# Kernel optimization log

Measured on AMD Instinct MI355X. Metric: run time of the kernel, lower is better.

Reference implementation:

```python
import jax, jax.numpy as jnp
import numpy as np
from jax import lax

B_J0 = 0.01   # config.b_j0
R_M = 1.0     # config.R_m
BETA = 1.8    # isAdapt=1 branch
GAMMA = 0.5   # config.gamma
LENS = 0.5    # config.lens
SCALE = 6.0   # config.scale
HIGHT = 0.15  # config.hight


def _gauss(x, mu, sigma):
    return jnp.exp(-(x - mu) ** 2 / (2.0 * sigma ** 2)) / jnp.sqrt(2.0 * jnp.pi) / sigma


@jax.custom_vjp
def spike_fn(x):
    return (x > 0).astype(x.dtype)

def _spike_fwd(x):
    return spike_fn(x), x

def _spike_bwd(x, g):
    # 'MG' multi-gaussian surrogate gradient from ActFun_adp.backward
    temp = (_gauss(x, 0.0, LENS) * (1.0 + HIGHT)
            - _gauss(x, LENS, SCALE * LENS) * HIGHT
            - _gauss(x, -LENS, SCALE * LENS) * HIGHT)
    return (g * temp * GAMMA,)

spike_fn.defvjp(_spike_fwd, _spike_bwd)


def setup_inputs() -> dict:
    key = jax.random.key(0)
    ks = jax.random.split(key, 20)
    B, T, I, H, O = 256, 250, 700, 128, 20
    def xav(k, shape):
        lim = jnp.sqrt(6.0 / (shape[0] + shape[1]))
        return jax.random.uniform(k, shape, jnp.float32, -lim, lim)
    def orth(k, n):
        a = jax.random.normal(k, (n, n), jnp.float32)
        q, r = jnp.linalg.qr(a)
        return q * jnp.sign(jnp.diag(r))[None, :]
    return {
        'input': jax.random.normal(ks[0], (B, T, I), jnp.float32),
        'A1_mask': jnp.ones((H, H), jnp.float32),
        'A2_mask': jnp.ones((H, H), jnp.float32),
        'W_ih1': xav(ks[1], (H, I)), 'b_ih1': jnp.zeros((H,), jnp.float32),
        'W_h1h1': orth(ks[2], H), 'b_h1h1': jnp.zeros((H,), jnp.float32),
        'W_h1h2': xav(ks[3], (H, H)), 'b_h1h2': jnp.zeros((H,), jnp.float32),
        'W_h2h2': orth(ks[4], H), 'b_h2h2': jnp.zeros((H,), jnp.float32),
        'W_h2o': xav(ks[5], (O, H)), 'b_h2o': jnp.zeros((O,), jnp.float32),
        'tau_adp_h1': 150.0 + 10.0 * jax.random.normal(ks[6], (H,), jnp.float32),
        'tau_adp_h2': 150.0 + 10.0 * jax.random.normal(ks[7], (H,), jnp.float32),
        'tau_m_h1': 20.0 + 5.0 * jax.random.normal(ks[8], (H,), jnp.float32),
        'tau_m_h2': 20.0 + 5.0 * jax.random.normal(ks[9], (H,), jnp.float32),
        'tau_m_o': 20.0 + 5.0 * jax.random.normal(ks[10], (O,), jnp.float32),
        'hid1_mem0': jax.random.uniform(ks[11], (B, H), jnp.float32),
        'hid2_mem0': jax.random.uniform(ks[12], (B, H), jnp.float32),
        'out_mem0': jax.random.uniform(ks[13], (B, O), jnp.float32),
    }


def reference(input, A1_mask, A2_mask,
              W_ih1, b_ih1, W_h1h1, b_h1h1, W_h1h2, b_h1h2,
              W_h2h2, b_h2h2, W_h2o, b_h2o,
              tau_adp_h1, tau_adp_h2, tau_m_h1, tau_m_h2, tau_m_o,
              hid1_mem0, hid2_mem0, out_mem0):
    B, T, _ = input.shape
    H = W_ih1.shape[0]
    O = W_h2o.shape[0]
    # time-constant decays (dt = 1), computed once
    a1 = jnp.exp(-1.0 / tau_m_h1)
    r1 = jnp.exp(-1.0 / tau_adp_h1)
    a2 = jnp.exp(-1.0 / tau_m_h2)
    r2 = jnp.exp(-1.0 / tau_adp_h2)
    ao = jnp.exp(-1.0 / tau_m_o)

    xT = jnp.swapaxes(input, 0, 1)  # [T, B, I]
    carry0 = (hid1_mem0, jnp.zeros((B, H), input.dtype), jnp.full((B, H), B_J0, input.dtype),
              hid2_mem0, jnp.zeros((B, H), input.dtype), jnp.full((B, H), B_J0, input.dtype),
              out_mem0, jnp.zeros((B, O), input.dtype))

    def step(carry, xs):
        x_t, t = xs
        h1m, h1s, b1, h2m, h2s, b2, om, acc = carry
        # layer 1: input + recurrent drive, adaptive threshold LIF update
        in1 = x_t @ W_ih1.T + b_ih1 + h1s @ W_h1h1.T + b_h1h1
        b1 = r1 * b1 + (1.0 - r1) * h1s
        Bth1 = B_J0 + BETA * b1
        h1m = h1m * a1 + (1.0 - a1) * R_M * in1 - Bth1 * h1s
        h1s = spike_fn(h1m - Bth1)
        # layer 2
        in2 = h1s @ W_h1h2.T + b_h1h2 + h2s @ W_h2h2.T + b_h2h2
        b2 = r2 * b2 + (1.0 - r2) * h2s
        Bth2 = B_J0 + BETA * b2
        h2m = h2m * a2 + (1.0 - a2) * R_M * in2 - Bth2 * h2s
        h2s = spike_fn(h2m - Bth2)
        # leaky-integrator readout (no spike)
        om = om * ao + (1.0 - ao) * R_M * (h2s @ W_h2o.T + b_h2o)
        # accumulate softmax only for t > 10
        acc = acc + jnp.where(t > 10, 1.0, 0.0) * jax.nn.softmax(om, axis=1)
        return (h1m, h1s, b1, h2m, h2s, b2, om, acc), None

    final, _ = lax.scan(step, carry0, (xT, jnp.arange(T)))
    output = final[-1]
    A_norm = jnp.sum(jnp.abs(W_h1h1)) + jnp.sum(jnp.abs(W_h2h2))
    return output, A_norm


if __name__ == '__main__':
    out = reference(**setup_inputs())
    print(out[0].shape, out[1])
```

## Files before the change

kernel.cpp:

```cpp
#include <hip/hip_runtime.h>
#include <hip/hip_bf16.h>
#include <stdint.h>

#define HN 128
#define TSTEPS 250
#define ON 20
#define GK 700
#define NKT 22

typedef _Float16 h2 __attribute__((ext_vector_type(2)));
typedef _Float16 h8 __attribute__((ext_vector_type(8)));
typedef float f4 __attribute__((ext_vector_type(4)));

__device__ __forceinline__ h2 bch_u(uint32_t u) { return __builtin_bit_cast(h2, u); }
__device__ __forceinline__ h2 bch_f(float f)    { return __builtin_bit_cast(h2, f); }
__device__ __forceinline__ float fdot2(h2 a, h2 b, float c) {
    return __builtin_amdgcn_fdot2(a, b, c, false);
}
__device__ __forceinline__ float pack2(float x, float y) {
    h2 p; p.x = (_Float16)x; p.y = (_Float16)y;
    return __builtin_bit_cast(float, p);
}
__device__ __forceinline__ uint32_t pack2u(float x, float y) {
    h2 p; p.x = (_Float16)x; p.y = (_Float16)y;
    return __builtin_bit_cast(uint32_t, p);
}

__global__ __launch_bounds__(256) void ff_gemm(const float* __restrict__ X,
                                               const float* __restrict__ W,
                                               const float* __restrict__ bias,
                                               float* __restrict__ out) {
    __shared__ __align__(16) uint32_t Xs[2][128][16];
    __shared__ __align__(16) uint32_t Ws[2][128][16];
    const int tid   = threadIdx.x;
    const int w     = tid >> 6;
    const int lane  = tid & 63;
    const int m0    = blockIdx.x * 128;
    const int srow  = tid & 127;
    const int shalf = tid >> 7;
    const int lr    = lane & 15;
    const int lg    = lane >> 4;

    f4 acc[2][8];
#pragma unroll
    for (int m = 0; m < 2; ++m)
#pragma unroll
        for (int n = 0; n < 8; ++n) acc[m][n] = (f4){0.f, 0.f, 0.f, 0.f};

    float4 x4[4], w4[4];

#define LOADT(t)                                                               \
    {                                                                          \
        const int k0 = (t) * 32 + shalf * 16;                                  \
        if ((t) < 21 || shalf == 0) {                                          \
            _Pragma("unroll")                                                  \
            for (int q = 0; q < 4; ++q) {                                      \
                x4[q] = *(const float4*)&X[(size_t)(m0 + srow) * GK + k0 + q * 4]; \
                w4[q] = *(const float4*)&W[(size_t)srow * GK + k0 + q * 4];    \
            }                                                                  \
        } else {       \
            _Pragma("unroll")                                                  \
            for (int q = 0; q < 3; ++q) {                                      \
                x4[q] = *(const float4*)&X[(size_t)(m0 + srow) * GK + k0 + q * 4]; \
                w4[q] = *(const float4*)&W[(size_t)srow * GK + k0 + q * 4];    \
            }                                                                  \
            x4[3] = (float4){0.f, 0.f, 0.f, 0.f};                              \
            w4[3] = (float4){0.f, 0.f, 0.f, 0.f};                              \
        }                                                                      \
    }
#define STORET(buf)                                                            \
    {                                                                          \
        _Pragma("unroll")                                                      \
        for (int q = 0; q < 4; ++q) {                                          \
            Xs[buf][srow][shalf * 8 + 2 * q]     = pack2u(x4[q].x, x4[q].y);   \
            Xs[buf][srow][shalf * 8 + 2 * q + 1] = pack2u(x4[q].z, x4[q].w);   \
            Ws[buf][srow][shalf * 8 + 2 * q]     = pack2u(w4[q].x, w4[q].y);   \
            Ws[buf][srow][shalf * 8 + 2 * q + 1] = pack2u(w4[q].z, w4[q].w);   \
        }                                                                      \
    }

    LOADT(0);
    STORET(0);
    __syncthreads();
    int cur = 0;
    for (int t = 0; t < NKT; ++t) {
        if (t + 1 < NKT) LOADT(t + 1);
        h8 a[2];
#pragma unroll
        for (int m = 0; m < 2; ++m) {
            const uint4 au = *(const uint4*)&Xs[cur][w * 32 + m * 16 + lr][lg * 4];
            a[m] = __builtin_bit_cast(h8, au);
        }
#pragma unroll
        for (int n = 0; n < 8; ++n) {
            const uint4 bu = *(const uint4*)&Ws[cur][n * 16 + lr][lg * 4];
            const h8 bf = __builtin_bit_cast(h8, bu);
            acc[0][n] = __builtin_amdgcn_mfma_f32_16x16x32_f16(a[0], bf, acc[0][n], 0, 0, 0);
            acc[1][n] = __builtin_amdgcn_mfma_f32_16x16x32_f16(a[1], bf, acc[1][n], 0, 0, 0);
        }
        if (t + 1 < NKT) STORET(cur ^ 1);
        __syncthreads();
        cur ^= 1;
    }

    float bv[8];
#pragma unroll
    for (int n = 0; n < 8; ++n) bv[n] = bias[n * 16 + lr];
#pragma unroll
    for (int m = 0; m < 2; ++m)
#pragma unroll
        for (int q = 0; q < 4; ++q) {
            const size_t row = (size_t)(m0 + w * 32 + m * 16 + lg * 4 + q);
#pragma unroll
            for (int n = 0; n < 8; ++n)
                out[row * HN + n * 16 + lr] = acc[m][n][q] + bv[n];
        }
#undef LOADT
#undef STORET
}

__device__ __forceinline__ float mv1h(const float4 (&WP)[16][HN],
                                      const uint4 (&sv)[16], int j) {
    float a0 = 0.f, a1 = 0.f, a2 = 0.f, a3 = 0.f;
#pragma unroll
    for (int t = 0; t < 16; ++t) {
        const float4 wl = WP[t][j];
        const uint4  s  = sv[t];
        a0 = fdot2(bch_f(wl.x), bch_u(s.x), a0);
        a1 = fdot2(bch_f(wl.y), bch_u(s.y), a1);
        a2 = fdot2(bch_f(wl.z), bch_u(s.z), a2);
        a3 = fdot2(bch_f(wl.w), bch_u(s.w), a3);
    }
    return (a0 + a1) + (a2 + a3);
}
__device__ __forceinline__ float mv1o(const float4 (&WP)[16][32],
                                      const uint4 (&sv)[16], int j) {
    float a0 = 0.f, a1 = 0.f, a2 = 0.f, a3 = 0.f;
#pragma unroll
    for (int t = 0; t < 16; ++t) {
        const float4 wl = WP[t][j];
        const uint4  s  = sv[t];
        a0 = fdot2(bch_f(wl.x), bch_u(s.x), a0);
        a1 = fdot2(bch_f(wl.y), bch_u(s.y), a1);
        a2 = fdot2(bch_f(wl.z), bch_u(s.z), a2);
        a3 = fdot2(bch_f(wl.w), bch_u(s.w), a3);
    }
    return (a0 + a1) + (a2 + a3);
}

#define LOADSPIKES(arr, buf, sv)                                               \
    {                                                                          \
        const uint4* _p = (const uint4*)&arr[buf][0];                          \
        _Pragma("unroll") for (int _t = 0; _t < 16; ++_t) sv[_t] = _p[_t];     \
    }

__global__ __launch_bounds__(512) void srnn_pipe8(
    const float* __restrict__ ff,
    const float* __restrict__ W_h1h1, const float* __restrict__ b_h1h1,
    const float* __restrict__ W_h1h2, const float* __restrict__ b_h1h2,
    const float* __restrict__ W_h2h2, const float* __restrict__ b_h2h2,
    const float* __restrict__ W_h2o,  const float* __restrict__ b_h2o,
    const float* __restrict__ tau_adp_h1, const float* __restrict__ tau_adp_h2,
    const float* __restrict__ tau_m_h1,   const float* __restrict__ tau_m_h2,
    const float* __restrict__ tau_m_o,
    const float* __restrict__ h1m0, const float* __restrict__ h2m0,
    const float* __restrict__ om0,
    float* __restrict__ out) {
    const int b    = blockIdx.x;
    const int tid  = threadIdx.x;
    const int w    = tid >> 6;
    const int lane = tid & 63;

    __shared__ float4 WPA[16][HN];
    __shared__ float4 WPB[16][HN];
    __shared__ float4 WPC[16][HN];
    __shared__ float4 WPO[16][32];
    __shared__ _Float16 s1h[2][HN];
    __shared__ _Float16 s2h[2][HN];
    __shared__ float pBbuf[2][HN];
    __shared__ float rdot_lds[2][32];

#pragma unroll
    for (int e = tid; e < 2048; e += 512) {
        const int t = e >> 7, j = e & 127;
        {
            const float* s = W_h1h1 + j * HN + t * 8;
            float4 x0 = *(const float4*)s, x1 = *(const float4*)(s + 4);
            float4 d; d.x = pack2(x0.x, x0.y); d.y = pack2(x0.z, x0.w);
            d.z = pack2(x1.x, x1.y); d.w = pack2(x1.z, x1.w);
            WPA[t][j] = d;
        }
        {
            const float* s = W_h1h2 + j * HN + t * 8;
            float4 x0 = *(const float4*)s, x1 = *(const float4*)(s + 4);
            float4 d; d.x = pack2(x0.x, x0.y); d.y = pack2(x0.z, x0.w);
            d.z = pack2(x1.x, x1.y); d.w = pack2(x1.z, x1.w);
            WPB[t][j] = d;
        }
        {
            const float* s = W_h2h2 + j * HN + t * 8;
            float4 x0 = *(const float4*)s, x1 = *(const float4*)(s + 4);
            float4 d; d.x = pack2(x0.x, x0.y); d.y = pack2(x0.z, x0.w);
            d.z = pack2(x1.x, x1.y); d.w = pack2(x1.z, x1.w);
            WPC[t][j] = d;
        }
    }
    {
        const int t = tid >> 5, j = tid & 31;
        float4 d = {0.f, 0.f, 0.f, 0.f};
        if (j < ON) {
            const float* s = W_h2o + j * HN + t * 8;
            float4 x0 = *(const float4*)s, x1 = *(const float4*)(s + 4);
            d.x = pack2(x0.x, x0.y); d.y = pack2(x0.z, x0.w);
            d.z = pack2(x1.x, x1.y); d.w = pack2(x1.z, x1.w);
        }
        WPO[t][j] = d;
    }
    if (tid < HN) {
        s1h[0][tid] = (_Float16)0; s1h[1][tid] = (_Float16)0;
        s2h[0][tid] = (_Float16)0; s2h[1][tid] = (_Float16)0;
    }
    __syncthreads();

    if (w < 2) {
        const int j = (w << 6) + lane;
        float h1m = h1m0[b * HN + j];
        const float a1 = expf(-1.f / tau_m_h1[j]);
        const float r1 = expf(-1.f / tau_adp_h1[j]);
        const float bi = b_h1h1[j];
        float b1 = 0.01f, s1p = 0.f;
        const float* fp = ff + (size_t)b * TSTEPS * HN + j;
        float fc = fp[0], fn = fp[HN];
        for (int i = 0; i < TSTEPS + 4; ++i) {
            if (i < TSTEPS) {
                const float f2 = (i + 2 < TSTEPS) ? fp[(size_t)(i + 2) * HN] : 0.f;
                uint4 sv[16];
                LOADSPIKES(s1h, (i + 1) & 1, sv);
                const float pA = mv1h(WPA, sv, j);
                b1 = r1 * b1 + (1.f - r1) * s1p;
                const float Bt = 0.01f + 1.8f * b1;
                h1m = h1m * a1 + (1.f - a1) * (fc + bi + pA) - Bt * s1p;
                s1p = (h1m - Bt > 0.f) ? 1.f : 0.f;
                s1h[i & 1][j] = (_Float16)s1p;
                fc = fn; fn = f2;
            }
            __syncthreads();
        }
    } else if (w < 4) {
        const int j = ((w - 2) << 6) + lane;
        for (int i = 0; i < TSTEPS + 4; ++i) {
            if (i >= 1 && i <= TSTEPS) {
                uint4 sv[16];
                LOADSPIKES(s1h, (i - 1) & 1, sv);
                pBbuf[(i - 1) & 1][j] = mv1h(WPB, sv, j);
            }
            __syncthreads();
        }
    } else if (w < 6) {
        const int j = ((w - 4) << 6) + lane;
        float h2m = h2m0[b * HN + j];
        const float a2 = expf(-1.f / tau_m_h2[j]);
        const float r2 = expf(-1.f / tau_adp_h2[j]);
        const float bi = b_h1h2[j] + b_h2h2[j];
        float b2v = 0.01f, s2p = 0.f;
        for (int i = 0; i < TSTEPS + 4; ++i) {
            if (i >= 2 && i <= TSTEPS + 1) {
                const int k2 = i - 2;
                uint4 sv[16];
                LOADSPIKES(s2h, (k2 + 1) & 1, sv);
                const float pC = mv1h(WPC, sv, j);
                const float in2 = pBbuf[k2 & 1][j] + pC + bi;
                b2v = r2 * b2v + (1.f - r2) * s2p;
                const float Bt = 0.01f + 1.8f * b2v;
                h2m = h2m * a2 + (1.f - a2) * in2 - Bt * s2p;
                s2p = (h2m - Bt > 0.f) ? 1.f : 0.f;
                s2h[k2 & 1][j] = (_Float16)s2p;
            }
            __syncthreads();
        }
    } else if (w == 6) {
        const int o = lane;
        for (int i = 0; i < TSTEPS + 4; ++i) {
            if (i >= 3 && i <= TSTEPS + 2 && o < ON) {
                const int k3 = i - 3;
                uint4 sv[16];
                LOADSPIKES(s2h, k3 & 1, sv);
                rdot_lds[k3 & 1][o] = mv1o(WPO, sv, o);
            }
            __syncthreads();
        }
    } else {
        const int o = lane;
        float om = 0.f, ao = 0.f, bo = 0.f, acc = 0.f;
        if (o < ON) {
            om = om0[b * ON + o];
            ao = expf(-1.f / tau_m_o[o]);
            bo = b_h2o[o];
        }
        for (int i = 0; i < TSTEPS + 4; ++i) {
            if (i >= 4) {
                const int k4 = i - 4;
                if (o < ON)
                    om = om * ao + (1.f - ao) * (rdot_lds[k4 & 1][o] + bo);
                float mx = (o < ON) ? om : -3.4e38f;
#pragma unroll
                for (int m = 16; m >= 1; m >>= 1)
                    mx = fmaxf(mx, __shfl_xor(mx, m));
                float e = (o < ON) ? __expf(om - mx) : 0.f;
                float den = e;
#pragma unroll
                for (int m = 16; m >= 1; m >>= 1)
                    den += __shfl_xor(den, m);
                if (o < ON && k4 > 10) acc += e / den;
            }
            __syncthreads();
        }
        if (o < ON) out[b * ON + o] = acc;
    }
}

__global__ void anorm_kernel(const float* __restrict__ W1,
                             const float* __restrict__ W2,
                             float* __restrict__ out) {
    __shared__ float red[256];
    float s = 0.f;
    for (int i = threadIdx.x; i < HN * HN; i += 256)
        s += fabsf(W1[i]) + fabsf(W2[i]);
    red[threadIdx.x] = s;
    __syncthreads();
    for (int off = 128; off > 0; off >>= 1) {
        if (threadIdx.x < off) red[threadIdx.x] += red[threadIdx.x + off];
        __syncthreads();
    }
    if (threadIdx.x == 0) out[256 * ON] = red[0];
}

extern "C" void kernel_launch(void* const* d_in, const int* in_sizes, int n_in,
                              void* d_out, int out_size, void* d_ws, size_t ws_size,
                              hipStream_t stream) {
    const float* input      = (const float*)d_in[0];
    const float* W_ih1      = (const float*)d_in[3];
    const float* b_ih1      = (const float*)d_in[4];
    const float* W_h1h1     = (const float*)d_in[5];
    const float* b_h1h1     = (const float*)d_in[6];
    const float* W_h1h2     = (const float*)d_in[7];
    const float* b_h1h2     = (const float*)d_in[8];
    const float* W_h2h2     = (const float*)d_in[9];
    const float* b_h2h2     = (const float*)d_in[10];
    const float* W_h2o      = (const float*)d_in[11];
    const float* b_h2o      = (const float*)d_in[12];
    const float* tau_adp_h1 = (const float*)d_in[13];
    const float* tau_adp_h2 = (const float*)d_in[14];
    const float* tau_m_h1   = (const float*)d_in[15];
    const float* tau_m_h2   = (const float*)d_in[16];
    const float* tau_m_o    = (const float*)d_in[17];
    const float* h1m0       = (const float*)d_in[18];
    const float* h2m0       = (const float*)d_in[19];
    const float* om0        = (const float*)d_in[20];

    float* out   = (float*)d_out;
    float* ffbuf = (float*)d_ws;

    anorm_kernel<<<1, 256, 0, stream>>>(W_h1h1, W_h2h2, out);
    ff_gemm<<<500, 256, 0, stream>>>(input, W_ih1, b_ih1, ffbuf);
    srnn_pipe8<<<256, 512, 0, stream>>>(ffbuf, W_h1h1, b_h1h1, W_h1h2, b_h1h2,
                                        W_h2h2, b_h2h2, W_h2o, b_h2o,
                                        tau_adp_h1, tau_adp_h2,
                                        tau_m_h1, tau_m_h2, tau_m_o,
                                        h1m0, h2m0, om0, out);
}
```

Measured before the change: 262.0 us.

## Quantize recurrent weights to int8 and pack spikes as bytes for sdot4

Recurrent and readout weights are quantized per row to int8 with a scale, and spike vectors are packed as bytes via wave shuffles. The matvecs then use sdot4 over 8 uint4 groups instead of fp16 fdot2 over 16. This halves the LDS traffic and the dot instruction count in the serial per-timestep critical path. It trades away accuracy: int8 weight rounding could flip spike decisions and change outputs beyond tolerance, and the prologue now does per-row absmax passes.

```diff
diff --git a/kernel.cpp b/kernel.cpp
--- a/kernel.cpp
+++ b/kernel.cpp
@@ -12,15 +12,6 @@
 typedef _Float16 h8 __attribute__((ext_vector_type(8)));
 typedef float f4 __attribute__((ext_vector_type(4)));
 
-__device__ __forceinline__ h2 bch_u(uint32_t u) { return __builtin_bit_cast(h2, u); }
-__device__ __forceinline__ h2 bch_f(float f)    { return __builtin_bit_cast(h2, f); }
-__device__ __forceinline__ float fdot2(h2 a, h2 b, float c) {
-    return __builtin_amdgcn_fdot2(a, b, c, false);
-}
-__device__ __forceinline__ float pack2(float x, float y) {
-    h2 p; p.x = (_Float16)x; p.y = (_Float16)y;
-    return __builtin_bit_cast(float, p);
-}
 __device__ __forceinline__ uint32_t pack2u(float x, float y) {
     h2 p; p.x = (_Float16)x; p.y = (_Float16)y;
     return __builtin_bit_cast(uint32_t, p);
@@ -58,7 +49,7 @@
                 x4[q] = *(const float4*)&X[(size_t)(m0 + srow) * GK + k0 + q * 4]; \
                 w4[q] = *(const float4*)&W[(size_t)srow * GK + k0 + q * 4];    \
             }                                                                  \
-        } else {       \
+        } else {                                                               \
             _Pragma("unroll")                                                  \
             for (int q = 0; q < 3; ++q) {                                      \
                 x4[q] = *(const float4*)&X[(size_t)(m0 + srow) * GK + k0 + q * 4]; \
@@ -119,42 +110,42 @@
 #undef STORET
 }
 
-__device__ __forceinline__ float mv1h(const float4 (&WP)[16][HN],
-                                      const uint4 (&sv)[16], int j) {
-    float a0 = 0.f, a1 = 0.f, a2 = 0.f, a3 = 0.f;
-#pragma unroll
-    for (int t = 0; t < 16; ++t) {
-        const float4 wl = WP[t][j];
-        const uint4  s  = sv[t];
-        a0 = fdot2(bch_f(wl.x), bch_u(s.x), a0);
-        a1 = fdot2(bch_f(wl.y), bch_u(s.y), a1);
-        a2 = fdot2(bch_f(wl.z), bch_u(s.z), a2);
-        a3 = fdot2(bch_f(wl.w), bch_u(s.w), a3);
-    }
-    return (a0 + a1) + (a2 + a3);
-}
-__device__ __forceinline__ float mv1o(const float4 (&WP)[16][32],
-                                      const uint4 (&sv)[16], int j) {
-    float a0 = 0.f, a1 = 0.f, a2 = 0.f, a3 = 0.f;
-#pragma unroll
-    for (int t = 0; t < 16; ++t) {
-        const float4 wl = WP[t][j];
-        const uint4  s  = sv[t];
-        a0 = fdot2(bch_f(wl.x), bch_u(s.x), a0);
-        a1 = fdot2(bch_f(wl.y), bch_u(s.y), a1);
-        a2 = fdot2(bch_f(wl.z), bch_u(s.z), a2);
-        a3 = fdot2(bch_f(wl.w), bch_u(s.w), a3);
-    }
-    return (a0 + a1) + (a2 + a3);
-}
-
-#define LOADSPIKES(arr, buf, sv)                                               \
+__device__ __forceinline__ int mvq(const uint4 (&W)[8][HN],
+                                   const uint4 (&sv)[8], int j) {
+    int a = 0;
+#pragma unroll
+    for (int g = 0; g < 8; ++g) {
+        const uint4 wq = W[g][j];
+        const uint4 sq = sv[g];
+        a = __builtin_amdgcn_sdot4((int)wq.x, (int)sq.x, a, false);
+        a = __builtin_amdgcn_sdot4((int)wq.y, (int)sq.y, a, false);
+        a = __builtin_amdgcn_sdot4((int)wq.z, (int)sq.z, a, false);
+        a = __builtin_amdgcn_sdot4((int)wq.w, (int)sq.w, a, false);
+    }
+    return a;
+}
+__device__ __forceinline__ int mvqo(const uint4 (&W)[8][32],
+                                    const uint4 (&sv)[8], int j) {
+    int a = 0;
+#pragma unroll
+    for (int g = 0; g < 8; ++g) {
+        const uint4 wq = W[g][j];
+        const uint4 sq = sv[g];
+        a = __builtin_amdgcn_sdot4((int)wq.x, (int)sq.x, a, false);
+        a = __builtin_amdgcn_sdot4((int)wq.y, (int)sq.y, a, false);
+        a = __builtin_amdgcn_sdot4((int)wq.z, (int)sq.z, a, false);
+        a = __builtin_amdgcn_sdot4((int)wq.w, (int)sq.w, a, false);
+    }
+    return a;
+}
+
+#define LOADQ(arr, buf, sv)                                                    \
     {                                                                          \
         const uint4* _p = (const uint4*)&arr[buf][0];                          \
-        _Pragma("unroll") for (int _t = 0; _t < 16; ++_t) sv[_t] = _p[_t];     \
-    }
-
-__global__ __launch_bounds__(512) void srnn_pipe8(
+        _Pragma("unroll") for (int _g = 0; _g < 8; ++_g) sv[_g] = _p[_g];      \
+    }
+
+__global__ __launch_bounds__(512) void srnn_pipe9(
     const float* __restrict__ ff,
     const float* __restrict__ W_h1h1, const float* __restrict__ b_h1h1,
     const float* __restrict__ W_h1h2, const float* __restrict__ b_h1h2,
@@ -171,59 +162,76 @@
     const int w    = tid >> 6;
     const int lane = tid & 63;
 
-    __shared__ float4 WPA[16][HN];
-    __shared__ float4 WPB[16][HN];
-    __shared__ float4 WPC[16][HN];
-    __shared__ float4 WPO[16][32];
-    __shared__ _Float16 s1h[2][HN];
-    __shared__ _Float16 s2h[2][HN];
+    __shared__ __align__(16) uint4 WQA[8][HN];
+    __shared__ __align__(16) uint4 WQB[8][HN];
+    __shared__ __align__(16) uint4 WQC[8][HN];
+    __shared__ __align__(16) uint4 WQO[8][32];
+    __shared__ float scA[HN], scB[HN], scC[HN], scO[32];
+    __shared__ __align__(16) uint32_t s1w[2][32];
+    __shared__ __align__(16) uint32_t s2w[2][32];
     __shared__ float pBbuf[2][HN];
     __shared__ float rdot_lds[2][32];
 
-#pragma unroll
-    for (int e = tid; e < 2048; e += 512) {
-        const int t = e >> 7, j = e & 127;
-        {
-            const float* s = W_h1h1 + j * HN + t * 8;
-            float4 x0 = *(const float4*)s, x1 = *(const float4*)(s + 4);
-            float4 d; d.x = pack2(x0.x, x0.y); d.y = pack2(x0.z, x0.w);
-            d.z = pack2(x1.x, x1.y); d.w = pack2(x1.z, x1.w);
-            WPA[t][j] = d;
-        }
-        {
-            const float* s = W_h1h2 + j * HN + t * 8;
-            float4 x0 = *(const float4*)s, x1 = *(const float4*)(s + 4);
-            float4 d; d.x = pack2(x0.x, x0.y); d.y = pack2(x0.z, x0.w);
-            d.z = pack2(x1.x, x1.y); d.w = pack2(x1.z, x1.w);
-            WPB[t][j] = d;
-        }
-        {
-            const float* s = W_h2h2 + j * HN + t * 8;
-            float4 x0 = *(const float4*)s, x1 = *(const float4*)(s + 4);
-            float4 d; d.x = pack2(x0.x, x0.y); d.y = pack2(x0.z, x0.w);
-            d.z = pack2(x1.x, x1.y); d.w = pack2(x1.z, x1.w);
-            WPC[t][j] = d;
-        }
-    }
-    {
-        const int t = tid >> 5, j = tid & 31;
-        float4 d = {0.f, 0.f, 0.f, 0.f};
-        if (j < ON) {
-            const float* s = W_h2o + j * HN + t * 8;
-            float4 x0 = *(const float4*)s, x1 = *(const float4*)(s + 4);
-            d.x = pack2(x0.x, x0.y); d.y = pack2(x0.z, x0.w);
-            d.z = pack2(x1.x, x1.y); d.w = pack2(x1.z, x1.w);
-        }
-        WPO[t][j] = d;
-    }
-    if (tid < HN) {
-        s1h[0][tid] = (_Float16)0; s1h[1][tid] = (_Float16)0;
-        s2h[0][tid] = (_Float16)0; s2h[1][tid] = (_Float16)0;
+    if (tid < 416) {
+        const int role = tid >> 7;
+        const int j    = tid & 127;
+        const bool isO = (role == 3);
+        const bool on  = !isO || (j < 32);
+        if (on) {
+            const float* src = nullptr;
+            bool valid = true;
+            if (!isO) {
+                src = (role == 0 ? W_h1h1 : role == 1 ? W_h1h2 : W_h2h2) + j * HN;
+            } else if (j < ON) {
+                src = W_h2o + j * HN;
+            } else {
+                valid = false;
+            }
+            float amax = 0.f;
+            if (valid) {
+#pragma unroll
+                for (int q = 0; q < 32; ++q) {
+                    float4 v = *(const float4*)&src[q * 4];
+                    amax = fmaxf(amax, fmaxf(fmaxf(fabsf(v.x), fabsf(v.y)),
+                                             fmaxf(fabsf(v.z), fabsf(v.w))));
+                }
+            }
+            const float qs = (valid && amax > 0.f) ? 127.f / amax : 0.f;
+#pragma unroll
+            for (int g = 0; g < 8; ++g) {
+                uint32_t u[4] = {0u, 0u, 0u, 0u};
+                if (valid) {
+#pragma unroll
+                    for (int e = 0; e < 4; ++e) {
+                        float4 v = *(const float4*)&src[g * 16 + e * 4];
+                        const int q0 = (int)rintf(v.x * qs), q1 = (int)rintf(v.y * qs);
+                        const int q2 = (int)rintf(v.z * qs), q3 = (int)rintf(v.w * qs);
+                        u[e] = (uint32_t)(q0 & 255) | ((uint32_t)(q1 & 255) << 8) |
+                               ((uint32_t)(q2 & 255) << 16) | ((uint32_t)(q3 & 255) << 24);
+                    }
+                }
+                uint4 w4; w4.x = u[0]; w4.y = u[1]; w4.z = u[2]; w4.w = u[3];
+                if (isO) WQO[g][j] = w4;
+                else if (role == 0) WQA[g][j] = w4;
+                else if (role == 1) WQB[g][j] = w4;
+                else WQC[g][j] = w4;
+            }
+            const float os = (valid && amax > 0.f) ? amax / 127.f : 0.f;
+            if (isO) scO[j] = os;
+            else if (role == 0) scA[j] = os;
+            else if (role == 1) scB[j] = os;
+            else scC[j] = os;
+        }
+    }
+    if (tid < 32) {
+        s1w[0][tid] = 0u; s1w[1][tid] = 0u;
+        s2w[0][tid] = 0u; s2w[1][tid] = 0u;
     }
     __syncthreads();
 
     if (w < 2) {
         const int j = (w << 6) + lane;
+        const float sA = scA[j];
         float h1m = h1m0[b * HN + j];
         const float a1 = expf(-1.f / tau_m_h1[j]);
         const float r1 = expf(-1.f / tau_adp_h1[j]);
@@ -234,30 +242,35 @@
         for (int i = 0; i < TSTEPS + 4; ++i) {
             if (i < TSTEPS) {
                 const float f2 = (i + 2 < TSTEPS) ? fp[(size_t)(i + 2) * HN] : 0.f;
-                uint4 sv[16];
-                LOADSPIKES(s1h, (i + 1) & 1, sv);
-                const float pA = mv1h(WPA, sv, j);
+                uint4 sv[8];
+                LOADQ(s1w, (i + 1) & 1, sv);
+                const float pA = sA * (float)mvq(WQA, sv, j);
                 b1 = r1 * b1 + (1.f - r1) * s1p;
                 const float Bt = 0.01f + 1.8f * b1;
                 h1m = h1m * a1 + (1.f - a1) * (fc + bi + pA) - Bt * s1p;
-                s1p = (h1m - Bt > 0.f) ? 1.f : 0.f;
-                s1h[i & 1][j] = (_Float16)s1p;
+                const int sp = (h1m - Bt > 0.f) ? 1 : 0;
+                s1p = (float)sp;
+                int pk = sp | (__shfl_down(sp, 1) << 8) |
+                         (__shfl_down(sp, 2) << 16) | (__shfl_down(sp, 3) << 24);
+                if ((lane & 3) == 0) s1w[i & 1][(w << 4) + (lane >> 2)] = (uint32_t)pk;
                 fc = fn; fn = f2;
             }
             __syncthreads();
         }
     } else if (w < 4) {
         const int j = ((w - 2) << 6) + lane;
+        const float sB = scB[j];
         for (int i = 0; i < TSTEPS + 4; ++i) {
             if (i >= 1 && i <= TSTEPS) {
-                uint4 sv[16];
-                LOADSPIKES(s1h, (i - 1) & 1, sv);
-                pBbuf[(i - 1) & 1][j] = mv1h(WPB, sv, j);
+                uint4 sv[8];
+                LOADQ(s1w, (i - 1) & 1, sv);
+                pBbuf[(i - 1) & 1][j] = sB * (float)mvq(WQB, sv, j);
             }
             __syncthreads();
         }
     } else if (w < 6) {
         const int j = ((w - 4) << 6) + lane;
+        const float sC = scC[j];
         float h2m = h2m0[b * HN + j];
         const float a2 = expf(-1.f / tau_m_h2[j]);
         const float r2 = expf(-1.f / tau_adp_h2[j]);
@@ -266,26 +279,30 @@
         for (int i = 0; i < TSTEPS + 4; ++i) {
             if (i >= 2 && i <= TSTEPS + 1) {
                 const int k2 = i - 2;
-                uint4 sv[16];
-                LOADSPIKES(s2h, (k2 + 1) & 1, sv);
-                const float pC = mv1h(WPC, sv, j);
+                uint4 sv[8];
+                LOADQ(s2w, (k2 + 1) & 1, sv);
+                const float pC = sC * (float)mvq(WQC, sv, j);
                 const float in2 = pBbuf[k2 & 1][j] + pC + bi;
                 b2v = r2 * b2v + (1.f - r2) * s2p;
                 const float Bt = 0.01f + 1.8f * b2v;
                 h2m = h2m * a2 + (1.f - a2) * in2 - Bt * s2p;
-                s2p = (h2m - Bt > 0.f) ? 1.f : 0.f;
-                s2h[k2 & 1][j] = (_Float16)s2p;
+                const int sp = (h2m - Bt > 0.f) ? 1 : 0;
+                s2p = (float)sp;
+                int pk = sp | (__shfl_down(sp, 1) << 8) |
+                         (__shfl_down(sp, 2) << 16) | (__shfl_down(sp, 3) << 24);
+                if ((lane & 3) == 0) s2w[k2 & 1][((w - 4) << 4) + (lane >> 2)] = (uint32_t)pk;
             }
             __syncthreads();
         }
     } else if (w == 6) {
         const int o = lane;
+        const float sO = (o < 32) ? scO[o] : 0.f;
         for (int i = 0; i < TSTEPS + 4; ++i) {
             if (i >= 3 && i <= TSTEPS + 2 && o < ON) {
                 const int k3 = i - 3;
-                uint4 sv[16];
-                LOADSPIKES(s2h, k3 & 1, sv);
-                rdot_lds[k3 & 1][o] = mv1o(WPO, sv, o);
+                uint4 sv[8];
+                LOADQ(s2w, k3 & 1, sv);
+                rdot_lds[k3 & 1][o] = sO * (float)mvqo(WQO, sv, o);
             }
             __syncthreads();
         }
@@ -363,7 +380,7 @@
 
     anorm_kernel<<<1, 256, 0, stream>>>(W_h1h1, W_h2h2, out);
     ff_gemm<<<500, 256, 0, stream>>>(input, W_ih1, b_ih1, ffbuf);
-    srnn_pipe8<<<256, 512, 0, stream>>>(ffbuf, W_h1h1, b_h1h1, W_h1h2, b_h1h2,
+    srnn_pipe9<<<256, 512, 0, stream>>>(ffbuf, W_h1h1, b_h1h1, W_h1h2, b_h1h2,
                                         W_h2h2, b_h2h2, W_h2o, b_h2o,
                                         tau_adp_h1, tau_adp_h2,
                                         tau_m_h1, tau_m_h2, tau_m_o,
```

Result: faster. 221.8 us (-15.4%).
